# Optimization experiments

Hardware: AMD Instinct MI355X
Metric: run time of the kernel (lower is better)

## Reference

```python
import jax, jax.numpy as jnp
import numpy as np

B = 1
T_DIM, H_DIM, W_DIM = 8, 24, 24          # video canvas (t, h, w)
TT, TH, TW = 2, 8, 8                      # tile sizes
WT, WH, WW = 6, 16, 16                    # window sizes (tokens)
HIDDEN = 1024
HEADS = 16
DH = HIDDEN // HEADS
SEQ = T_DIM * H_DIM * W_DIM               # 4608
NT, NH, NW = T_DIM // TT, H_DIM // TH, W_DIM // TW   # tile grid (4,3,3)
N_TILES = NT * NH * NW                    # 36
TILE = TT * TH * TW                       # 128


def _gather_indices():
    # STA tile mask: kv tile allowed iff |clamp(q_tile, k//2, n-1-k//2) - kv_tile| <= k//2 per axis.
    # Due to the clamp, every query tile attends to exactly the same number of kv tiles,
    # so the block-sparse pattern is a dense gather of shape [N_TILES, K].
    def axis(n, kernel_tiles):
        half = kernel_tiles // 2
        c = np.clip(np.arange(n), half, n - 1 - half)
        return c[:, None] + np.arange(-half, half + 1)[None, :]  # [n, 2*half+1]
    ts = axis(NT, WT // TT)
    hs = axis(NH, WH // TH)
    ws = axis(NW, WW // TW)
    idx = (ts[:, None, None, :, None, None] * NH
           + hs[None, :, None, None, :, None]) * NW \
          + ws[None, None, :, None, None, :]
    return idx.reshape(N_TILES, -1).astype(np.int32)  # [N_TILES, K]


def setup_inputs() -> dict:
    key = jax.random.key(0)
    k1, k2, k3, k4, k5 = jax.random.split(key, 5)
    s = 0.02
    return {
        "hidden_states": jax.random.normal(k1, (B, SEQ, HIDDEN), jnp.float32),
        "q_w": jax.random.normal(k2, (HIDDEN, HIDDEN), jnp.float32) * s,
        "k_w": jax.random.normal(k3, (HIDDEN, HIDDEN), jnp.float32) * s,
        "v_w": jax.random.normal(k4, (HIDDEN, HIDDEN), jnp.float32) * s,
        "o_w": jax.random.normal(k5, (HIDDEN, HIDDEN), jnp.float32) * s,
    }


def _tileize(x):
    # [B, S, HEADS*DH] -> [B, HEADS, N_TILES, TILE, DH] in (t,h,w) tile-major order
    x = x.reshape(B, NT, TT, NH, TH, NW, TW, HEADS, DH)
    x = x.transpose(0, 7, 1, 3, 5, 2, 4, 6, 8)
    return x.reshape(B, HEADS, N_TILES, TILE, DH)


def _untileize(x):
    # [B, HEADS, N_TILES, TILE, DH] -> [B, S, HEADS*DH]
    x = x.reshape(B, HEADS, NT, NH, NW, TT, TH, TW, DH)
    x = x.transpose(0, 2, 5, 3, 6, 4, 7, 1, 8)
    return x.reshape(B, SEQ, HEADS * DH)


def reference(hidden_states, q_w, k_w, v_w, o_w):
    q = _tileize(hidden_states @ q_w.T)
    k = _tileize(hidden_states @ k_w.T)
    v = _tileize(hidden_states @ v_w.T)
    idx = jnp.asarray(_gather_indices())          # [N_TILES, K] (static)
    kk = k[:, :, idx]                              # [B, H, N_TILES, K, TILE, DH]
    vv = v[:, :, idx]
    K = idx.shape[1]
    kk = kk.reshape(B, HEADS, N_TILES, K * TILE, DH)
    vv = vv.reshape(B, HEADS, N_TILES, K * TILE, DH)
    scale = 1.0 / np.sqrt(DH).astype(np.float32)
    scores = jnp.einsum('bhnqd,bhnkd->bhnqk', q * scale, kk)  # [B,H,nT,TILE,K*TILE]
    attn = jax.nn.softmax(scores, axis=-1)
    out = jnp.einsum('bhnqk,bhnkd->bhnqd', attn, vv)
    return _untileize(out) @ o_w.T
```

## Files before the change

### kernel.cpp

```cpp
#include <hip/hip_runtime.h>
#include <math.h>

#define HID 1024
#define NHEADS 16
#define NTILES 36
#define HEADSZ (36*128*64)
#define LOG2E 1.4426950408889634f
#define PLSTRIDE 73728

typedef unsigned short u16;
typedef unsigned int u32;
typedef __attribute__((ext_vector_type(8))) u16 ushort8v;
typedef __attribute__((ext_vector_type(8))) __bf16 bf16x8;
typedef __attribute__((ext_vector_type(16))) float f32x16;
typedef __attribute__((ext_vector_type(4))) u32 u32x4;

__device__ __forceinline__ u32 cvt_pk_bf16(float lo, float hi) {
  u32 r;
  asm("v_cvt_pk_bf16_f32 %0, %1, %2" : "=v"(r) : "v"(lo), "v"(hi));
  return r;
}
__device__ __forceinline__ void permlane32_swap(u32 &a, u32 &b) {
  asm volatile("v_permlane32_swap_b32 %0, %1" : "+v"(a), "+v"(b));
}
__device__ __forceinline__ void gld_lds16(const void* g, void* l) {
  __builtin_amdgcn_global_load_lds((const __attribute__((address_space(1))) u32*)g,
                                   (__attribute__((address_space(3))) u32*)l, 16, 0, 0);
}
__device__ __forceinline__ f32x16 mfma32(bf16x8 a, bf16x8 b, f32x16 c) {
  return __builtin_amdgcn_mfma_f32_32x32x16_bf16(a, b, c, 0, 0, 0);
}
__device__ __forceinline__ u16 bf16r(float x) {
  u32 b = __builtin_bit_cast(u32, x);
  b += 0x7fff + ((b >> 16) & 1);
  return (u16)(b >> 16);
}
__device__ __forceinline__ float bf2f(u16 v) {
  return __builtin_bit_cast(float, (u32)v << 16);
}

struct CastJob { const float* src[5]; u16* dst[5]; int n[5]; };

__global__ __launch_bounds__(256)
void cast_bf16(CastJob j) {
  const int w = blockIdx.y;
  const int n = j.n[w];
  const int i = (blockIdx.x * 256 + threadIdx.x) * 8;
  if (i >= n) return;
  const float4 v0 = *reinterpret_cast<const float4*>(j.src[w] + i);
  const float4 v1 = *reinterpret_cast<const float4*>(j.src[w] + i + 4);
  u32x4 o;
  o.x = cvt_pk_bf16(v0.x, v0.y);
  o.y = cvt_pk_bf16(v0.z, v0.w);
  o.z = cvt_pk_bf16(v1.x, v1.y);
  o.w = cvt_pk_bf16(v1.z, v1.w);
  *reinterpret_cast<u32x4*>(j.dst[w] + i) = o;
}

template<int AMODE, int CMODE, bool QKV, bool DBUF>
__global__ __launch_bounds__(256)
void gemm_mfma(const u16* __restrict__ A, const u16* __restrict__ B,
               void* __restrict__ Cv, float alpha)
{
    __shared__ __align__(16) u16 sm[DBUF ? 2 : 1][2][8192];

    const int tid = threadIdx.x;
    const int wv = tid >> 6, l = tid & 63;
    const int l31 = l & 31, hi = l >> 5;
    const int wm = wv >> 1, wn = wv & 1;
    const int by = blockIdx.y;
    const int n0 = blockIdx.x * 128;
    const float av = (QKV && n0 >= 1024) ? 1.0f : alpha;

    const int tt = by / 9, rem = by % 9, th = rem / 3, tw = rem % 3;
    const int tilebase = tt * 1152 + th * 192 + tw * 8;

    const int lrow = l >> 3;
    const int lslot = l & 7;
    const int sg = (lslot ^ lrow) * 8;
    const u16* aptr[4];
    const u16* bptr[4];
#pragma unroll
    for (int i = 0; i < 4; ++i) {
        const int row = (wv * 4 + i) * 8 + lrow;
        if (AMODE == 0) {
            const int s = tilebase + (row >> 6) * 576 + ((row >> 3) & 7) * 24 + (row & 7);
            aptr[i] = A + (size_t)s * HID + sg;
        } else {
            aptr[i] = A + (size_t)(by * 128 + row) * 64 + sg;
        }
        bptr[i] = B + (size_t)(n0 + row) * HID + sg;
    }

    auto stage = [&](int buf, int kc) {
#pragma unroll
        for (int i = 0; i < 4; ++i) {
            const u16* ga = (AMODE == 0) ? (aptr[i] + kc)
                                         : (aptr[i] + (size_t)(kc >> 6) * HEADSZ);
            gld_lds16(ga, &sm[buf][0][(wv * 4 + i) * 512]);
            gld_lds16(bptr[i] + kc, &sm[buf][1][(wv * 4 + i) * 512]);
        }
    };

    f32x16 acc[2][2];
#pragma unroll
    for (int mb = 0; mb < 2; ++mb)
#pragma unroll
        for (int nb = 0; nb < 2; ++nb)
#pragma unroll
            for (int i = 0; i < 16; ++i) acc[mb][nb][i] = 0.f;

    auto compute = [&](int buf) {
        __builtin_amdgcn_s_setprio(1);
#pragma unroll
        for (int kk = 0; kk < 4; ++kk) {
            bf16x8 af[2], bfr[2];
#pragma unroll
            for (int mb = 0; mb < 2; ++mb) {
                const int row = wm * 64 + mb * 32 + l31;
                af[mb] = *reinterpret_cast<const bf16x8*>(
                    &sm[buf][0][row * 64 + (((kk * 2 + hi) ^ (row & 7)) * 8)]);
            }
#pragma unroll
            for (int nb = 0; nb < 2; ++nb) {
                const int row = wn * 64 + nb * 32 + l31;
                bfr[nb] = *reinterpret_cast<const bf16x8*>(
                    &sm[buf][1][row * 64 + (((kk * 2 + hi) ^ (row & 7)) * 8)]);
            }
#pragma unroll
            for (int mb = 0; mb < 2; ++mb)
#pragma unroll
                for (int nb = 0; nb < 2; ++nb)
                    acc[mb][nb] = mfma32(af[mb], bfr[nb], acc[mb][nb]);
        }
        __builtin_amdgcn_s_setprio(0);
    };

    if (DBUF) {
        stage(0, 0);
        __syncthreads();
        int cur = 0;
        for (int kc = 0; kc < HID; kc += 64) {
            if (kc + 64 < HID) stage(cur ^ 1, kc + 64);
            compute(cur);
            __syncthreads();
            cur ^= 1;
        }
    } else {
        for (int kc = 0; kc < HID; kc += 64) {
            __syncthreads();
            stage(0, kc);
            __syncthreads();
            compute(0);
        }
    }

    if (CMODE == 0) {
        float* C = (float*)Cv;
#pragma unroll
        for (int mb = 0; mb < 2; ++mb)
#pragma unroll
            for (int r = 0; r < 16; ++r) {
                const int m = wm * 64 + mb * 32 + (r & 3) + 8 * (r >> 2) + 4 * hi;
                const int s = tilebase + (m >> 6) * 576 + ((m >> 3) & 7) * 24 + (m & 7);
#pragma unroll
                for (int nb = 0; nb < 2; ++nb) {
                    const int n = n0 + wn * 64 + nb * 32 + l31;
                    C[(size_t)s * HID + n] = acc[mb][nb][r] * av;
                }
            }
    } else {
        u16* C = (u16*)Cv;
#pragma unroll
        for (int mb = 0; mb < 2; ++mb)
#pragma unroll
            for (int rq = 0; rq < 4; ++rq) {
                const int mbase = wm * 64 + mb * 32 + 8 * rq + 4 * hi;
#pragma unroll
                for (int nb = 0; nb < 2; ++nb) {
                    const int n = n0 + wn * 64 + nb * 32 + l31;
                    const int head = n >> 6, dh = n & 63;
                    if (QKV && head >= 32) {
                        u32 w0 = cvt_pk_bf16(acc[mb][nb][rq * 4 + 0], acc[mb][nb][rq * 4 + 1]);
                        u32 w1 = cvt_pk_bf16(acc[mb][nb][rq * 4 + 2], acc[mb][nb][rq * 4 + 3]);
                        *reinterpret_cast<uint2*>(C + (size_t)head * HEADSZ +
                            (size_t)by * 8192 + (mbase >> 3) * 512 + (dh << 3) +
                            (mbase & 7)) = make_uint2(w0, w1);
                    } else {
#pragma unroll
                        for (int j = 0; j < 4; ++j) {
                            const int m = mbase + j;
                            C[(size_t)head * HEADSZ + (size_t)(by * 128 + m) * 64 + dh] =
                                bf16r(acc[mb][nb][rq * 4 + j] * av);
                        }
                    }
                }
            }
    }
}

__global__ __launch_bounds__(256, 4)
void attn_mfma(const u16* __restrict__ Q, const u16* __restrict__ K,
               const u16* __restrict__ Vt, u16* __restrict__ pO0,
               u16* __restrict__ pO1, float* __restrict__ pl)
{
    __shared__ u16 sm[2][4096];

    const int tid = threadIdx.x;
    const int wave = tid >> 6;
    const int lane = tid & 63;
    const int l31 = lane & 31;
    const int hi  = lane >> 5;

    const int logical = (blockIdx.x & 7) * 144 + (blockIdx.x >> 3);
    const int p  = logical & 1;
    const int bt = logical >> 1;
    const int tl = bt % NTILES;
    const int hd = bt / NTILES;
    const size_t headbase = (size_t)hd * HEADSZ;

    const u16* Qg = Q + headbase + (size_t)tl * 8192;
    const u16* Kh = K + headbase;
    const u16* Vh = Vt + headbase;

    bf16x8 qf[4];
    {
        const u16* qrow = Qg + (wave * 32 + l31) * 64 + hi * 8;
#pragma unroll
        for (int ks = 0; ks < 4; ++ks)
            qf[ks] = *reinterpret_cast<const bf16x8*>(qrow + ks * 16);
    }

    const int base_t = (min(max(tl / 9, 1), 2) - 1) * 9;

    const int srow = lane >> 3;
    const int slot = lane & 7;

    auto stage = [&](int i, int bi) {
        const int kt = base_t + i;
        const u16* Kg = Kh + (size_t)kt * 8192 + p * 4096;
        u16* dk = &sm[bi][0];
#pragma unroll
        for (int q = 0; q < 2; ++q) {
            const int seg = wave * 2 + q;
            const int key = seg * 8 + srow;
            gld_lds16(Kg + key * 64 + ((slot ^ (key & 7)) * 8), dk + seg * 512);
        }
    };

    f32x16 accO0, accO1;
#pragma unroll
    for (int i = 0; i < 16; ++i) { accO0[i] = 0.f; accO1[i] = 0.f; }
    float lsum = 0.f;

    stage(0, 0);
    __syncthreads();

    for (int i = 0; i < 27; ++i) {
        const int cur = i & 1;
        if (i + 1 < 27) stage(i + 1, cur ^ 1);
        const u16* Ksb = &sm[cur][0];
        const u16* Vg = Vh + (size_t)(base_t + i) * 8192;

#pragma unroll
        for (int c = 0; c < 2; ++c) {
            bf16x8 vf[2][2];
#pragma unroll
            for (int k2 = 0; k2 < 2; ++k2) {
                const int chunk = 8 * p + 4 * c + 2 * k2 + hi;
                const u16* vb = Vg + chunk * 512 + l31 * 8;
                vf[k2][0] = *reinterpret_cast<const bf16x8*>(vb);
                vf[k2][1] = *reinterpret_cast<const bf16x8*>(vb + 256);
            }

            f32x16 s;
#pragma unroll
            for (int i2 = 0; i2 < 16; ++i2) s[i2] = 0.f;
            const int kr = c * 32 + l31;
            __builtin_amdgcn_s_setprio(1);
#pragma unroll
            for (int ks = 0; ks < 4; ++ks) {
                bf16x8 a = *reinterpret_cast<const bf16x8*>(
                    Ksb + kr * 64 + (((2 * ks + hi) ^ (kr & 7)) * 8));
                s = mfma32(a, qf[ks], s);
            }
            __builtin_amdgcn_s_setprio(0);

#pragma unroll
            for (int i2 = 0; i2 < 16; ++i2) s[i2] = __builtin_amdgcn_exp2f(s[i2]);

            float ps = 0.f;
#pragma unroll
            for (int i2 = 0; i2 < 16; ++i2) ps += s[i2];
            lsum += ps;

            bf16x8 pb[2];
            {
                u32 a0 = cvt_pk_bf16(s[0], s[1]);
                u32 a1 = cvt_pk_bf16(s[2], s[3]);
                u32 b0 = cvt_pk_bf16(s[4], s[5]);
                u32 b1 = cvt_pk_bf16(s[6], s[7]);
                permlane32_swap(a0, b0);
                permlane32_swap(a1, b1);
                u32x4 w; w.x = a0; w.y = a1; w.z = b0; w.w = b1;
                pb[0] = __builtin_bit_cast(bf16x8, w);
                u32 c0 = cvt_pk_bf16(s[8], s[9]);
                u32 c1 = cvt_pk_bf16(s[10], s[11]);
                u32 d0 = cvt_pk_bf16(s[12], s[13]);
                u32 d1 = cvt_pk_bf16(s[14], s[15]);
                permlane32_swap(c0, d0);
                permlane32_swap(c1, d1);
                u32x4 w2; w2.x = c0; w2.y = c1; w2.z = d0; w2.w = d1;
                pb[1] = __builtin_bit_cast(bf16x8, w2);
            }

            __builtin_amdgcn_s_setprio(1);
#pragma unroll
            for (int k2 = 0; k2 < 2; ++k2) {
                accO0 = mfma32(vf[k2][0], pb[k2], accO0);
                accO1 = mfma32(vf[k2][1], pb[k2], accO1);
            }
            __builtin_amdgcn_s_setprio(0);
        }
        __syncthreads();
    }

    lsum += __shfl_xor(lsum, 32);

    u16* Ob = (p ? pO1 : pO0) + ((size_t)bt * 128 + wave * 32 + l31) * 64;
#pragma unroll
    for (int t = 0; t < 4; ++t) {
        u32 p0 = cvt_pk_bf16(accO0[4 * t], accO0[4 * t + 1]);
        u32 p1 = cvt_pk_bf16(accO0[4 * t + 2], accO0[4 * t + 3]);
        *reinterpret_cast<uint2*>(Ob + t * 8 + 4 * hi) = make_uint2(p0, p1);
        u32 q0 = cvt_pk_bf16(accO1[4 * t], accO1[4 * t + 1]);
        u32 q1 = cvt_pk_bf16(accO1[4 * t + 2], accO1[4 * t + 3]);
        *reinterpret_cast<uint2*>(Ob + 32 + t * 8 + 4 * hi) = make_uint2(q0, q1);
    }
    if (hi == 0) pl[p * PLSTRIDE + bt * 128 + wave * 32 + l31] = lsum;
}

__global__ __launch_bounds__(256)
void merge_attn(const u16* __restrict__ pO0, const u16* __restrict__ pO1,
                const float* __restrict__ pl, u16* __restrict__ O)
{
    const int b = blockIdx.x;
    const int tid = threadIdx.x;
    const int row = tid >> 1;
    const int d0 = (tid & 1) * 32;
    const size_t rbase = ((size_t)b * 128 + row) * 64 + d0;
    const float inv = 1.f / (pl[b * 128 + row] + pl[PLSTRIDE + b * 128 + row]);
#pragma unroll
    for (int g = 0; g < 4; ++g) {
        ushort8v a = *reinterpret_cast<const ushort8v*>(pO0 + rbase + g * 8);
        ushort8v c = *reinterpret_cast<const ushort8v*>(pO1 + rbase + g * 8);
        u32 w[4];
#pragma unroll
        for (int h = 0; h < 4; ++h) {
            float f0 = (bf2f(a[2 * h])     + bf2f(c[2 * h]))     * inv;
            float f1 = (bf2f(a[2 * h + 1]) + bf2f(c[2 * h + 1])) * inv;
            w[h] = cvt_pk_bf16(f0, f1);
        }
        u32x4 st; st.x = w[0]; st.y = w[1]; st.z = w[2]; st.w = w[3];
        *reinterpret_cast<u32x4*>(O + rbase + g * 8) = st;
    }
}

extern "C" void kernel_launch(void* const* d_in, const int* in_sizes, int n_in,
                              void* d_out, int out_size, void* d_ws, size_t ws_size,
                              hipStream_t stream) {
    const float* hs = (const float*)d_in[0];
    const float* qw = (const float*)d_in[1];
    const float* kw = (const float*)d_in[2];
    const float* vw = (const float*)d_in[3];
    const float* ow = (const float*)d_in[4];
    float* out = (float*)d_out;

    const size_t TSZ = (size_t)NHEADS * HEADSZ;
    const size_t WSZ = (size_t)HID * HID;
    u16* hsb = (u16*)d_ws;
    u16* wqb = hsb + TSZ;
    u16* wkb = wqb + WSZ;
    u16* wvb = wkb + WSZ;
    u16* wob = wvb + WSZ;
    u16* qb  = wob + WSZ;
    u16* kb  = qb + TSZ;
    u16* vt  = kb + TSZ;
    u16* pO0 = hsb;
    u16* pO1 = vt + TSZ;
    float* pl = (float*)(pO1 + TSZ);
    u16* aob = (u16*)(pl + 2 * PLSTRIDE);

    CastJob cj;
    cj.src[0] = hs; cj.dst[0] = hsb; cj.n[0] = (int)TSZ;
    cj.src[1] = qw; cj.dst[1] = wqb; cj.n[1] = (int)WSZ;
    cj.src[2] = kw; cj.dst[2] = wkb; cj.n[2] = (int)WSZ;
    cj.src[3] = vw; cj.dst[3] = wvb; cj.n[3] = (int)WSZ;
    cj.src[4] = ow; cj.dst[4] = wob; cj.n[4] = (int)WSZ;
    cast_bf16<<<dim3(2304, 5), 256, 0, stream>>>(cj);

    gemm_mfma<0, 1, true, true><<<dim3(24, 36), 256, 0, stream>>>(hsb, wqb, qb, 0.125f * LOG2E);
    attn_mfma<<<NHEADS * NTILES * 2, 256, 0, stream>>>(qb, kb, vt, pO0, pO1, pl);
    merge_attn<<<NHEADS * NTILES, 256, 0, stream>>>(pO0, pO1, pl, aob);
    gemm_mfma<1, 0, false, true><<<dim3(8, 36), 256, 0, stream>>>(aob, wob, out, 1.0f);
}
```

Baseline: 156.8 us.

## Drop split-KV attention and merge kernel; each block processes full KV range

Instead of splitting each query tile's KV range into two halves across two blocks and merging the partial outputs in a separate kernel, each block now loops over all 54 half-tiles and normalizes its output directly by the reciprocal row sum. This removes the merge launch, the partial-output and row-sum global traffic, and the extra workspace. In exchange the grid is halved to 576 blocks, which may underfill the GPU's compute units and lengthen each block's serial loop.

```diff
diff --git a/kernel.cpp b/kernel.cpp
--- a/kernel.cpp
+++ b/kernel.cpp
@@ -6,7 +6,6 @@
 #define NTILES 36
 #define HEADSZ (36*128*64)
 #define LOG2E 1.4426950408889634f
-#define PLSTRIDE 73728
 
 typedef unsigned short u16;
 typedef unsigned int u32;
@@ -201,8 +200,7 @@
 
 __global__ __launch_bounds__(256, 4)
 void attn_mfma(const u16* __restrict__ Q, const u16* __restrict__ K,
-               const u16* __restrict__ Vt, u16* __restrict__ pO0,
-               u16* __restrict__ pO1, float* __restrict__ pl)
+               const u16* __restrict__ Vt, u16* __restrict__ O)
 {
     __shared__ u16 sm[2][4096];
 
@@ -212,9 +210,7 @@
     const int l31 = lane & 31;
     const int hi  = lane >> 5;
 
-    const int logical = (blockIdx.x & 7) * 144 + (blockIdx.x >> 3);
-    const int p  = logical & 1;
-    const int bt = logical >> 1;
+    const int bt = (blockIdx.x & 7) * 72 + (blockIdx.x >> 3);
     const int tl = bt % NTILES;
     const int hd = bt / NTILES;
     const size_t headbase = (size_t)hd * HEADSZ;
@@ -236,9 +232,9 @@
     const int srow = lane >> 3;
     const int slot = lane & 7;
 
-    auto stage = [&](int i, int bi) {
-        const int kt = base_t + i;
-        const u16* Kg = Kh + (size_t)kt * 8192 + p * 4096;
+    auto stage = [&](int st, int bi) {
+        const int kt = base_t + (st >> 1);
+        const u16* Kg = Kh + (size_t)kt * 8192 + (st & 1) * 4096;
         u16* dk = &sm[bi][0];
 #pragma unroll
         for (int q = 0; q < 2; ++q) {
@@ -256,18 +252,19 @@
     stage(0, 0);
     __syncthreads();
 
-    for (int i = 0; i < 27; ++i) {
-        const int cur = i & 1;
-        if (i + 1 < 27) stage(i + 1, cur ^ 1);
+    for (int st = 0; st < 54; ++st) {
+        const int cur = st & 1;
+        if (st + 1 < 54) stage(st + 1, cur ^ 1);
         const u16* Ksb = &sm[cur][0];
-        const u16* Vg = Vh + (size_t)(base_t + i) * 8192;
+        const int half = st & 1;
+        const u16* Vg = Vh + (size_t)(base_t + (st >> 1)) * 8192;
 
 #pragma unroll
         for (int c = 0; c < 2; ++c) {
             bf16x8 vf[2][2];
 #pragma unroll
             for (int k2 = 0; k2 < 2; ++k2) {
-                const int chunk = 8 * p + 4 * c + 2 * k2 + hi;
+                const int chunk = 8 * half + 4 * c + 2 * k2 + hi;
                 const u16* vb = Vg + chunk * 512 + l31 * 8;
                 vf[k2][0] = *reinterpret_cast<const bf16x8*>(vb);
                 vf[k2][1] = *reinterpret_cast<const bf16x8*>(vb + 256);
@@ -326,43 +323,17 @@
     }
 
     lsum += __shfl_xor(lsum, 32);
-
-    u16* Ob = (p ? pO1 : pO0) + ((size_t)bt * 128 + wave * 32 + l31) * 64;
+    const float inv = __builtin_amdgcn_rcpf(lsum);
+
+    u16* Ob = O + ((size_t)bt * 128 + wave * 32 + l31) * 64;
 #pragma unroll
     for (int t = 0; t < 4; ++t) {
-        u32 p0 = cvt_pk_bf16(accO0[4 * t], accO0[4 * t + 1]);
-        u32 p1 = cvt_pk_bf16(accO0[4 * t + 2], accO0[4 * t + 3]);
+        u32 p0 = cvt_pk_bf16(accO0[4 * t] * inv, accO0[4 * t + 1] * inv);
+        u32 p1 = cvt_pk_bf16(accO0[4 * t + 2] * inv, accO0[4 * t + 3] * inv);
         *reinterpret_cast<uint2*>(Ob + t * 8 + 4 * hi) = make_uint2(p0, p1);
-        u32 q0 = cvt_pk_bf16(accO1[4 * t], accO1[4 * t + 1]);
-        u32 q1 = cvt_pk_bf16(accO1[4 * t + 2], accO1[4 * t + 3]);
+        u32 q0 = cvt_pk_bf16(accO1[4 * t] * inv, accO1[4 * t + 1] * inv);
+        u32 q1 = cvt_pk_bf16(accO1[4 * t + 2] * inv, accO1[4 * t + 3] * inv);
         *reinterpret_cast<uint2*>(Ob + 32 + t * 8 + 4 * hi) = make_uint2(q0, q1);
-    }
-    if (hi == 0) pl[p * PLSTRIDE + bt * 128 + wave * 32 + l31] = lsum;
-}
-
-__global__ __launch_bounds__(256)
-void merge_attn(const u16* __restrict__ pO0, const u16* __restrict__ pO1,
-                const float* __restrict__ pl, u16* __restrict__ O)
-{
-    const int b = blockIdx.x;
-    const int tid = threadIdx.x;
-    const int row = tid >> 1;
-    const int d0 = (tid & 1) * 32;
-    const size_t rbase = ((size_t)b * 128 + row) * 64 + d0;
-    const float inv = 1.f / (pl[b * 128 + row] + pl[PLSTRIDE + b * 128 + row]);
-#pragma unroll
-    for (int g = 0; g < 4; ++g) {
-        ushort8v a = *reinterpret_cast<const ushort8v*>(pO0 + rbase + g * 8);
-        ushort8v c = *reinterpret_cast<const ushort8v*>(pO1 + rbase + g * 8);
-        u32 w[4];
-#pragma unroll
-        for (int h = 0; h < 4; ++h) {
-            float f0 = (bf2f(a[2 * h])     + bf2f(c[2 * h]))     * inv;
-            float f1 = (bf2f(a[2 * h + 1]) + bf2f(c[2 * h + 1])) * inv;
-            w[h] = cvt_pk_bf16(f0, f1);
-        }
-        u32x4 st; st.x = w[0]; st.y = w[1]; st.z = w[2]; st.w = w[3];
-        *reinterpret_cast<u32x4*>(O + rbase + g * 8) = st;
     }
 }
 
@@ -386,10 +357,7 @@
     u16* qb  = wob + WSZ;
     u16* kb  = qb + TSZ;
     u16* vt  = kb + TSZ;
-    u16* pO0 = hsb;
-    u16* pO1 = vt + TSZ;
-    float* pl = (float*)(pO1 + TSZ);
-    u16* aob = (u16*)(pl + 2 * PLSTRIDE);
+    u16* aob = hsb;
 
     CastJob cj;
     cj.src[0] = hs; cj.dst[0] = hsb; cj.n[0] = (int)TSZ;
@@ -400,7 +368,6 @@
     cast_bf16<<<dim3(2304, 5), 256, 0, stream>>>(cj);
 
     gemm_mfma<0, 1, true, true><<<dim3(24, 36), 256, 0, stream>>>(hsb, wqb, qb, 0.125f * LOG2E);
-    attn_mfma<<<NHEADS * NTILES * 2, 256, 0, stream>>>(qb, kb, vt, pO0, pO1, pl);
-    merge_attn<<<NHEADS * NTILES, 256, 0, stream>>>(pO0, pO1, pl, aob);
+    attn_mfma<<<NHEADS * NTILES, 256, 0, stream>>>(qb, kb, vt, aob);
     gemm_mfma<1, 0, false, true><<<dim3(8, 36), 256, 0, stream>>>(aob, wob, out, 1.0f);
 }
```

Result: no change. 158.1 us (+0.8%).
